# Kernel tuning notes

Hardware: AMD Instinct MI355X
Metric: run time of the kernel (lower is better)

The kernel has to match this reference:

```python
import jax, jax.numpy as jnp
import numpy as np
import math

BLOCK = 4      # block_size
N_HEADS = 8
DIM = 512
COND = 512
B = 2
HWU = 32       # h = w = u
NN = 7         # 'cross' neighbors


def _layernorm(x, w, eps=1e-5):
    mu = x.mean(-1, keepdims=True)
    var = ((x - mu) ** 2).mean(-1, keepdims=True)
    return (x - mu) * jax.lax.rsqrt(var + eps) * w


def _modulate(x, shift, scale):
    return x * (1.0 + scale) + shift


def _rotate_half(x):
    x1, x2 = jnp.split(x, 2, axis=-1)
    return jnp.concatenate([-x2, x1], axis=-1)


def _rot(x, cos, sin):
    return x * cos + _rotate_half(x) * sin


def setup_inputs() -> dict:
    key = jax.random.key(0)
    ks = jax.random.split(key, 16)
    h = w = u = HWU
    S = h * w * u
    dh = DIM // N_HEADS
    P = BLOCK ** 3
    ib = HWU // BLOCK                       # blocks per axis = 8
    nb = ib ** 3                            # 512 blocks per batch

    x = jax.random.normal(ks[0], (B, S, DIM), jnp.float32)
    c = jax.random.normal(ks[1], (B, COND), jnp.float32)

    # proper rotary tables over P block-local positions
    inv = 1.0 / (10000.0 ** (np.arange(0, dh, 2, dtype=np.float32) / dh))
    f = np.arange(P, dtype=np.float32)[:, None] * inv[None, :]
    emb = np.concatenate([f, f], axis=-1)          # [P, dh]
    cos = jnp.asarray(np.cos(emb))[None, :, None, :]
    sin = jnp.asarray(np.sin(emb))[None, :, None, :]

    # neighbor indices (cross pattern) on the block grid, mirroring get_neighbor_indices
    grid = np.stack(np.meshgrid(np.arange(B), np.arange(ib), np.arange(ib), np.arange(ib), indexing='ij'), axis=-1)
    shifts = np.array([[0, 0, 0, 0], [0, 0, -1, 0], [0, -1, 0, 0], [0, 0, 0, -1],
                       [0, 0, 1, 0], [0, 1, 0, 0], [0, 0, 0, 1]])
    nbr = grid[..., None, :] + shifts[None, None, None, None, :, :]
    nbr[..., 1:] = np.clip(nbr[..., 1:], 0, ib - 1)
    flat = (nbr[..., 0] * ib * ib * ib + nbr[..., 1] * ib * ib
            + nbr[..., 2] * ib + nbr[..., 3]).reshape(B * nb, NN)
    # every other block is 'nonzero' -> Nsel = 512
    nonzero_blocks = np.arange(0, B * nb, 2, dtype=np.int64)
    nonzero_blocks_neighbor = flat[nonzero_blocks].reshape(-1).astype(np.int64)

    s = 0.02
    params = dict(
        norm1_w=jnp.ones((DIM,), jnp.float32),
        qkv_w=s * jax.random.normal(ks[2], (3 * DIM, DIM), jnp.float32),
        out_w=s * jax.random.normal(ks[3], (DIM, DIM), jnp.float32),
        norm2_w=jnp.ones((DIM,), jnp.float32),
        mlp_w1=s * jax.random.normal(ks[4], (4 * DIM, DIM), jnp.float32),
        mlp_b1=jnp.zeros((4 * DIM,), jnp.float32),
        mlp_w2=s * jax.random.normal(ks[5], (DIM, 4 * DIM), jnp.float32),
        mlp_b2=jnp.zeros((DIM,), jnp.float32),
        adaln_w=s * jax.random.normal(ks[6], (6 * DIM, COND), jnp.float32),
        adaln_b=jnp.zeros((6 * DIM,), jnp.float32),
        kv_empty=s * jax.random.normal(ks[7], (1, P, 2 * DIM), jnp.float32),
    )
    return dict(x=x, c=c, cos_q=cos, sin_q=sin, cos_k=cos, sin_k=sin,
                nonzero_blocks=jnp.asarray(nonzero_blocks),
                nonzero_blocks_neighbor=jnp.asarray(nonzero_blocks_neighbor),
                h=h, w=w, u=u, **params)


def reference(x, c, cos_q, sin_q, cos_k, sin_k, nonzero_blocks, nonzero_blocks_neighbor,
              h, w, u, norm1_w, qkv_w, out_w, norm2_w, mlp_w1, mlp_b1, mlp_w2, mlp_b2,
              adaln_w, adaln_b, kv_empty):
    Bx, S, D = x.shape
    bs = BLOCK
    ix, iy, iz = h // bs, w // bs, u // bs
    nb = ix * iy * iz
    P = bs ** 3
    dh = D // N_HEADS
    Nsel = nonzero_blocks.shape[0]

    def transform(t):
        t = t.reshape(Bx, ix, bs, iy, bs, iz, bs, D)
        return t.transpose(0, 1, 3, 5, 2, 4, 6, 7).reshape(Bx, nb, P, D)

    def inverse_transform(t):
        t = t.reshape(Bx, ix, iy, iz, bs, bs, bs, D)
        return t.transpose(0, 1, 4, 2, 5, 3, 6, 7).reshape(Bx, S, D)

    mods = (c @ adaln_w.T + adaln_b)[:, None, :]         # [B,1,6D]
    shift_msa, scale_msa, gate_msa, shift_mlp, scale_mlp, gate_mlp = jnp.split(mods, 6, axis=-1)

    x_skip = x
    xm = _modulate(_layernorm(x, norm1_w), shift_msa, scale_msa)
    xb = transform(xm).reshape(Bx * nb, P, D)
    x_sel = xb[nonzero_blocks]                            # [Nsel,P,D]

    qkv = x_sel @ qkv_w.T                                 # [Nsel,P,3D]
    q, k, v = jnp.split(qkv, 3, axis=-1)
    k_e, v_e = jnp.split(kv_empty, 2, axis=-1)            # [1,P,D]
    k_full = jnp.broadcast_to(k_e, (Bx * nb, P, D)).at[nonzero_blocks].set(k)
    v_full = jnp.broadcast_to(v_e, (Bx * nb, P, D)).at[nonzero_blocks].set(v)
    kn = k_full[nonzero_blocks_neighbor]                  # [Nsel*NN,P,D]
    vn = v_full[nonzero_blocks_neighbor]

    qh = _rot(q.reshape(Nsel, P, N_HEADS, dh), cos_q, sin_q)
    kh = _rot(kn.reshape(Nsel * NN, P, N_HEADS, dh), cos_k, sin_k)
    kh = kh.reshape(Nsel, NN * P, N_HEADS, dh)
    vh = vn.reshape(Nsel, NN * P, N_HEADS, dh)

    scores = jnp.einsum('bqhd,bkhd->bhqk', qh, kh) / math.sqrt(dh)
    attn = jax.nn.softmax(scores, axis=-1)
    out = jnp.einsum('bhqk,bkhd->bqhd', attn, vh).reshape(Nsel, P, D)

    xz = jnp.zeros((Bx * nb, P, D), out.dtype).at[nonzero_blocks].set(out)
    x_attn = inverse_transform(xz.reshape(Bx, nb, P, D))
    x1 = x_skip + gate_msa * (x_attn @ out_w.T)

    x2 = _modulate(_layernorm(x1, norm2_w), shift_mlp, scale_mlp)
    mlp = jax.nn.gelu(x2 @ mlp_w1.T + mlp_b1, approximate=True) @ mlp_w2.T + mlp_b2
    return x1 + gate_mlp * mlp
```

## Files before the change

### kernel.cpp

```cpp
#include <hip/hip_runtime.h>
#include <cstdint>
#include <cstddef>

typedef unsigned short u16;
typedef __attribute__((ext_vector_type(8))) __bf16 bf16x8;
typedef __attribute__((ext_vector_type(4))) float f32x4;

typedef __attribute__((address_space(1))) const void GAS;
typedef __attribute__((address_space(3))) void LAS;

__device__ __forceinline__ void gld_lds16(const void* g, void* l) {
  __builtin_amdgcn_global_load_lds((GAS*)g, (LAS*)l, 16, 0, 0);
}

__device__ __forceinline__ u16 f2bf(float f) {
  union { float f; unsigned u; } x; x.f = f;
  unsigned r = x.u + 0x7FFFu + ((x.u >> 16) & 1u);
  return (u16)(r >> 16);
}
__device__ __forceinline__ float bf2f(u16 s) {
  union { unsigned u; float f; } x; x.u = ((unsigned)s) << 16;
  return x.f;
}
__device__ __forceinline__ f32x4 mfma16(bf16x8 a, bf16x8 b, f32x4 c) {
  return __builtin_amdgcn_mfma_f32_16x16x32_bf16(a, b, c, 0, 0, 0);
}


__global__ void selmap_k(const int* __restrict__ nzb, int* __restrict__ map) {
  int t = threadIdx.x;
  map[t] = -1;
  __syncthreads();
  if (t < 512) map[nzb[t]] = t;
}

__global__ __launch_bounds__(256) void castw_k(const float* __restrict__ in,
                                               u16* __restrict__ out, int n4) {
  int i = blockIdx.x * 256 + threadIdx.x;
  if (i >= n4) return;
  float4 v = ((const float4*)in)[i];
  u16 o[4] = {f2bf(v.x), f2bf(v.y), f2bf(v.z), f2bf(v.w)};
  ((uint2*)out)[i] = *(uint2*)o;
}

__global__ __launch_bounds__(256) void adaln_k(const float* __restrict__ c,
    const float* __restrict__ w, const float* __restrict__ b, float* __restrict__ mods) {
  int j = blockIdx.x * 256 + threadIdx.x;
  int bt = blockIdx.y;
  const float4* cr = (const float4*)(c + bt * 512);
  const float4* wr = (const float4*)(w + (size_t)j * 512);
  float s = 0.f;
  #pragma unroll 4
  for (int k = 0; k < 128; ++k) {
    float4 a = wr[k], q = cr[k];
    s += a.x * q.x + a.y * q.y + a.z * q.z + a.w * q.w;
  }
  mods[bt * 3072 + j] = s + b[j];
}

__global__ __launch_bounds__(256) void kvempty_k(const float* __restrict__ kve,
    const float* __restrict__ cT, const float* __restrict__ sT,
    u16* __restrict__ kempty, u16* __restrict__ vTempty) {
  int T = blockIdx.x * 256 + threadIdx.x;
  int h = T >> 12, p = (T >> 6) & 63, d = T & 63;
  float kv = kve[p * 1024 + h * 64 + d];
  float pv = kve[p * 1024 + h * 64 + (d ^ 32)];
  float cs = cT[p * 64 + d], sn = sT[p * 64 + d];
  float r = kv * cs + ((d < 32) ? -pv : pv) * sn;
  kempty[(h * 64 + p) * 64 + d] = f2bf(r);
  vTempty[(h * 64 + d) * 64 + p] = f2bf(kve[p * 1024 + 512 + h * 64 + d]);
}


__global__ __launch_bounds__(256) void ln1_k(const float* __restrict__ x,
    const float* __restrict__ nw, const float* __restrict__ mods,
    const int* __restrict__ nzb, u16* __restrict__ xm) {
  int row = blockIdx.x * 4 + (threadIdx.x >> 6);
  int t = threadIdx.x & 63;
  int sel = row >> 6, p = row & 63;
  int g = nzb[sel];
  int bt = g >> 9, blk = g & 511;
  int s = (blk >> 6) * 4096 + (p >> 4) * 1024 + ((blk >> 3) & 7) * 128
        + ((p >> 2) & 3) * 32 + (blk & 7) * 4 + (p & 3);
  const float* src = x + ((size_t)bt * 32768 + s) * 512;
  int d0 = t * 8;
  float4 a = *(const float4*)(src + d0);
  float4 b = *(const float4*)(src + d0 + 4);
  float v[8] = {a.x, a.y, a.z, a.w, b.x, b.y, b.z, b.w};
  float sum = 0.f, sq = 0.f;
  #pragma unroll
  for (int j = 0; j < 8; ++j) { sum += v[j]; sq += v[j] * v[j]; }
  #pragma unroll
  for (int m = 1; m < 64; m <<= 1) {
    sum += __shfl_xor(sum, m, 64);
    sq  += __shfl_xor(sq, m, 64);
  }
  float mean = sum * (1.f / 512.f);
  float var = sq * (1.f / 512.f) - mean * mean;
  float rstd = rsqrtf(var + 1e-5f);
  const float* mb = mods + bt * 3072;
  u16 o[8];
  #pragma unroll
  for (int j = 0; j < 8; ++j) {
    int d = d0 + j;
    float xn = (v[j] - mean) * rstd * nw[d];
    o[j] = f2bf(xn * (1.f + mb[512 + d]) + mb[d]);
  }
  *(uint4*)(xm + (size_t)row * 512 + d0) = *(uint4*)o;
}


template <int EPI>
__global__ __launch_bounds__(512, 2) void gemm256(const u16* __restrict__ A,
    const u16* __restrict__ W, int M, int N, int K, void* __restrict__ outp,
    const float* __restrict__ bias, const u16* __restrict__ x1,
    const float* __restrict__ mods, int rowOff, int NB) {
  __shared__ u16 L[65536];
  const int nwg = gridDim.x;
  const int cpx = nwg >> 3;
  const int tile = ((int)blockIdx.x & 7) * cpx + ((int)blockIdx.x >> 3);
  const int bm = (tile / NB) * 256, bn = (tile % NB) * 256;
  const int tid = threadIdx.x;
  const int w = tid >> 6, l = tid & 63, lr = l & 15, lg = l >> 4;
  const int wr = w >> 2, wc = w & 3;

  const u16* ga[4];
  const u16* gb[4];
  #pragma unroll
  for (int i = 0; i < 4; ++i) {
    int s = i * 512 + tid;
    int r = s >> 3, c = (s & 7) ^ (r & 7);
    ga[i] = A + (size_t)(bm + r) * K + c * 8;
    gb[i] = W + (size_t)(bn + r) * K + c * 8;
  }

  f32x4 acc[8][4];
  #pragma unroll
  for (int i = 0; i < 8; ++i)
    #pragma unroll
    for (int j = 0; j < 4; ++j) acc[i][j] = (f32x4){0.f, 0.f, 0.f, 0.f};

  auto STAGE = [&](int kt, int buf) {
    u16* lb = L + buf * 32768;
    #pragma unroll
    for (int i = 0; i < 4; ++i) {
      gld_lds16(ga[i] + (size_t)kt * 64, lb + (i * 512 + tid) * 8);
      gld_lds16(gb[i] + (size_t)kt * 64, lb + 16384 + (i * 512 + tid) * 8);
    }
  };

  auto COMPUTE = [&](int buf) {
    const u16* LA = L + buf * 32768;
    const u16* LB = LA + 16384;
    bf16x8 bf[4][2];
    #pragma unroll
    for (int nf = 0; nf < 4; ++nf) {
      int Rb = wc * 64 + nf * 16 + lr;
      const u16* pb = LB + Rb * 64;
      int sw = Rb & 7;
      bf[nf][0] = *(const bf16x8*)(pb + ((lg ^ sw) << 3));
      bf[nf][1] = *(const bf16x8*)(pb + (((lg + 4) ^ sw) << 3));
    }
    __builtin_amdgcn_s_setprio(1);
    #pragma unroll
    for (int mf = 0; mf < 8; ++mf) {
      int Ra = wr * 128 + mf * 16 + lr;
      const u16* pa = LA + Ra * 64;
      int sw = Ra & 7;
      bf16x8 a0 = *(const bf16x8*)(pa + ((lg ^ sw) << 3));
      bf16x8 a1 = *(const bf16x8*)(pa + (((lg + 4) ^ sw) << 3));
      #pragma unroll
      for (int nf = 0; nf < 4; ++nf) {
        acc[mf][nf] = mfma16(a0, bf[nf][0], acc[mf][nf]);
        acc[mf][nf] = mfma16(a1, bf[nf][1], acc[mf][nf]);
      }
    }
    __builtin_amdgcn_s_setprio(0);
  };

  const int NT = K >> 6;
  STAGE(0, 0);
  for (int t = 0; t < NT - 1; ++t) {
    STAGE(t + 1, (t + 1) & 1);
    asm volatile("s_waitcnt vmcnt(8)" ::: "memory");
    __builtin_amdgcn_s_barrier();
    asm volatile("" ::: "memory");
    COMPUTE(t & 1);
    asm volatile("" ::: "memory");
    __builtin_amdgcn_s_barrier();
  }
  asm volatile("s_waitcnt vmcnt(0)" ::: "memory");
  __builtin_amdgcn_s_barrier();
  asm volatile("" ::: "memory");
  COMPUTE((NT - 1) & 1);

  const int row0 = bm + wr * 128, col0 = bn + wc * 64;
  #pragma unroll
  for (int mf = 0; mf < 8; ++mf) {
    #pragma unroll
    for (int nf = 0; nf < 4; ++nf) {
      #pragma unroll
      for (int j = 0; j < 4; ++j) {
        int row = row0 + mf * 16 + lg * 4 + j;
        int col = col0 + nf * 16 + lr;
        float v = acc[mf][nf][j];
        if constexpr (EPI == 0) {
          ((u16*)outp)[(size_t)row * N + col] = f2bf(v);
        } else if constexpr (EPI == 1) {
          ((float*)outp)[(size_t)row * N + col] = v;
        } else if constexpr (EPI == 2) {
          v += bias[col];
          float z = 1.5957691216057308f * (v + 0.044715f * v * v * v);
          float t = 1.f - 2.f / (1.f + __expf(z));
          ((u16*)outp)[(size_t)row * N + col] = f2bf(0.5f * v * (1.f + t));
        } else {
          v += bias[col];
          int grow = rowOff + row;
          int bt = grow >> 15;
          float gate = mods[bt * 3072 + 2560 + col];
          ((float*)outp)[(size_t)grow * 512 + col] =
              bf2f(x1[(size_t)grow * 512 + col]) + gate * v;
        }
      }
    }
  }
}


__global__ __launch_bounds__(256) void ropepack_k(const u16* __restrict__ qkv,
    const float* __restrict__ cq, const float* __restrict__ sq,
    const float* __restrict__ ck, const float* __restrict__ sk,
    u16* __restrict__ qb, u16* __restrict__ kb) {
  int T = blockIdx.x * 256 + threadIdx.x;
  int row = T >> 7, oct = T & 127;
  int c0 = oct * 8;
  int sel = row >> 6, p = row & 63;
  int isk = (c0 >= 512);
  int chn = c0 & 511;
  int h = chn >> 6, d0 = chn & 63;
  int lower = (d0 < 32);
  const u16* base = qkv + (size_t)row * 1536 + (isk ? 512 : 0) + h * 64;
  u16 vm[8], vp[8];
  *(uint4*)vm = *(const uint4*)(base + d0);
  *(uint4*)vp = *(const uint4*)(base + (d0 ^ 32));
  const float* cT = (isk ? ck : cq) + p * 64 + d0;
  const float* sT = (isk ? sk : sq) + p * 64 + d0;
  float scale = isk ? 1.f : 0.125f;
  u16 o[8];
  #pragma unroll
  for (int j = 0; j < 8; ++j) {
    float a = bf2f(vm[j]), b = bf2f(vp[j]);
    float r = a * cT[j] + (lower ? -b : b) * sT[j];
    o[j] = f2bf(r * scale);
  }
  u16* dst = (isk ? kb : qb) + (((size_t)sel * 8 + h) * 64 + p) * 64 + d0;
  *(uint4*)dst = *(uint4*)o;
}


__global__ __launch_bounds__(256) void vtrans_k(const u16* __restrict__ qkv,
                                                u16* __restrict__ vT) {
  __shared__ u16 tb[64 * 65];
  int sel = blockIdx.x >> 3, h = blockIdx.x & 7;
  int tid = threadIdx.x;
  int p = tid >> 2, q16 = (tid & 3) * 16;
  const u16* src = qkv + (size_t)(sel * 64 + p) * 1536 + 1024 + h * 64 + q16;
  u16 ld[16];
  *(uint4*)&ld[0] = *(const uint4*)src;
  *(uint4*)&ld[8] = *(const uint4*)(src + 8);
  #pragma unroll
  for (int j = 0; j < 16; ++j) tb[p * 65 + q16 + j] = ld[j];
  __syncthreads();
  int d = tid >> 2, po = (tid & 3) * 16;
  u16 o[16];
  #pragma unroll
  for (int j = 0; j < 16; ++j) o[j] = tb[(po + j) * 65 + d];
  u16* dst = vT + (((size_t)sel * 8 + h) * 64 + d) * 64 + po;
  *(uint4*)dst = *(uint4*)&o[0];
  *(uint4*)(dst + 8) = *(uint4*)&o[8];
}


__global__ __launch_bounds__(256, 4) void attn_k(const u16* __restrict__ qbuf,
    const u16* __restrict__ kfull, const u16* __restrict__ vT,
    const u16* __restrict__ kempty, const u16* __restrict__ vTempty,
    const int* __restrict__ nbrs, const int* __restrict__ selmap,
    u16* __restrict__ attnout) {
  __shared__ u16 KB[2][4096];
  __shared__ u16 Pl[4][16][72];
  int bid = blockIdx.x;
  int swz = (bid & 7) * 512 + (bid >> 3);
  int sel = swz >> 3, h = swz & 7;
  int tid = threadIdx.x;
  int w = tid >> 6, l = tid & 63, lr = l & 15, lg = l >> 4;

  int mmv[7];
  #pragma unroll
  for (int n = 0; n < 7; ++n) mmv[n] = selmap[nbrs[sel * 7 + n]];

  const u16* qg = qbuf + (((size_t)sel * 8 + h) * 64 + w * 16) * 64;
  bf16x8 qf0 = *(const bf16x8*)(qg + lr * 64 + lg * 8);
  bf16x8 qf1 = *(const bf16x8*)(qg + lr * 64 + 32 + lg * 8);

  int srow = tid >> 3;
  int soff = srow * 64 + (((tid & 7) ^ (srow & 7)) << 3);
  size_t hoff = (size_t)h * 4096;

  {
    const u16* kp = (mmv[0] >= 0) ? kfull + (size_t)mmv[0] * 32768 + hoff
                                  : kempty + hoff;
    gld_lds16(kp + soff, &KB[0][w * 512]);
    gld_lds16(kp + soff + 2048, &KB[0][2048 + w * 512]);
  }

  f32x4 o[4];
  float mrun[4], lrun[4];
  #pragma unroll
  for (int ct = 0; ct < 4; ++ct) o[ct] = (f32x4){0.f, 0.f, 0.f, 0.f};
  #pragma unroll
  for (int r = 0; r < 4; ++r) { mrun[r] = -1e30f; lrun[r] = 0.f; }

  #pragma unroll
  for (int n = 0; n < 7; ++n) {
    if (n < 6) {
      const u16* kp = (mmv[n + 1] >= 0) ? kfull + (size_t)mmv[n + 1] * 32768 + hoff
                                        : kempty + hoff;
      int b = (n + 1) & 1;
      gld_lds16(kp + soff, &KB[b][w * 512]);
      gld_lds16(kp + soff + 2048, &KB[b][2048 + w * 512]);
      asm volatile("s_waitcnt vmcnt(2)" ::: "memory");
    } else {
      asm volatile("s_waitcnt vmcnt(0)" ::: "memory");
    }
    __builtin_amdgcn_s_barrier();
    __builtin_amdgcn_sched_barrier(0);

    const u16* kl = &KB[n & 1][0];
    const u16* vp = (mmv[n] >= 0) ? vT + (size_t)mmv[n] * 32768 + hoff
                                  : vTempty + hoff;
    f32x4 s4[4];
    int xr = lr & 7;
    #pragma unroll
    for (int ct = 0; ct < 4; ++ct) {
      int row = ct * 16 + lr;
      bf16x8 b0 = *(const bf16x8*)(kl + row * 64 + ((lg ^ xr) << 3));
      bf16x8 b1 = *(const bf16x8*)(kl + row * 64 + (((lg + 4) ^ xr) << 3));
      f32x4 z = (f32x4){0.f, 0.f, 0.f, 0.f};
      z = mfma16(qf0, b0, z);
      z = mfma16(qf1, b1, z);
      s4[ct] = z;
    }
    float rmax[4], sc[4], rs[4];
    #pragma unroll
    for (int r = 0; r < 4; ++r)
      rmax[r] = fmaxf(fmaxf(s4[0][r], s4[1][r]), fmaxf(s4[2][r], s4[3][r]));
    #pragma unroll
    for (int r = 0; r < 4; ++r) {
      #pragma unroll
      for (int ms = 1; ms < 16; ms <<= 1)
        rmax[r] = fmaxf(rmax[r], __shfl_xor(rmax[r], ms, 64));
      float mn = fmaxf(mrun[r], rmax[r]);
      sc[r] = __expf(mrun[r] - mn);
      mrun[r] = mn;
      rs[r] = 0.f;
    }
    #pragma unroll
    for (int ct = 0; ct < 4; ++ct)
      #pragma unroll
      for (int r = 0; r < 4; ++r) {
        float e = __expf(s4[ct][r] - mrun[r]);
        s4[ct][r] = e;
        rs[r] += e;
      }
    #pragma unroll
    for (int r = 0; r < 4; ++r) {
      #pragma unroll
      for (int ms = 1; ms < 16; ms <<= 1) rs[r] += __shfl_xor(rs[r], ms, 64);
      lrun[r] = lrun[r] * sc[r] + rs[r];
    }
    #pragma unroll
    for (int ct = 0; ct < 4; ++ct)
      #pragma unroll
      for (int r = 0; r < 4; ++r) o[ct][r] *= sc[r];
    #pragma unroll
    for (int ct = 0; ct < 4; ++ct)
      #pragma unroll
      for (int r = 0; r < 4; ++r)
        Pl[w][lg * 4 + r][ct * 16 + lr] = f2bf(s4[ct][r]);
    asm volatile("s_waitcnt lgkmcnt(0)" ::: "memory");
    __builtin_amdgcn_sched_barrier(0);
    bf16x8 pa0 = *(const bf16x8*)&Pl[w][lr][lg * 8];
    bf16x8 pa1 = *(const bf16x8*)&Pl[w][lr][32 + lg * 8];
    #pragma unroll
    for (int ct = 0; ct < 4; ++ct) {
      bf16x8 v0 = *(const bf16x8*)(vp + (ct * 16 + lr) * 64 + lg * 8);
      bf16x8 v1 = *(const bf16x8*)(vp + (ct * 16 + lr) * 64 + 32 + lg * 8);
      o[ct] = mfma16(pa0, v0, o[ct]);
      o[ct] = mfma16(pa1, v1, o[ct]);
    }
    asm volatile("" ::: "memory");
    __builtin_amdgcn_s_barrier();
    __builtin_amdgcn_sched_barrier(0);
  }

  float inv[4];
  #pragma unroll
  for (int r = 0; r < 4; ++r) inv[r] = 1.f / lrun[r];
  #pragma unroll
  for (int ct = 0; ct < 4; ++ct)
    #pragma unroll
    for (int r = 0; r < 4; ++r) {
      int p = w * 16 + lg * 4 + r;
      int d = ct * 16 + lr;
      attnout[((size_t)sel * 64 + p) * 512 + h * 64 + d] = f2bf(o[ct][r] * inv[r]);
    }
}


__global__ __launch_bounds__(256) void x1ln2_k(const float* __restrict__ x,
    const float* __restrict__ opout, const int* __restrict__ selmap,
    const float* __restrict__ mods, const float* __restrict__ nw,
    u16* __restrict__ x1, u16* __restrict__ x2) {
  int row = blockIdx.x * 4 + (threadIdx.x >> 6);
  int t = threadIdx.x & 63;
  int bt = row >> 15, s = row & 32767;
  int i1 = s >> 12, p1 = (s >> 10) & 3, i2 = (s >> 7) & 7,
      p2 = (s >> 5) & 3, i3 = (s >> 2) & 7, p3 = s & 3;
  int blk = (((i1 << 3) | i2) << 3) | i3;
  int m = selmap[(bt << 9) | blk];
  int d0 = t * 8;
  const float* src = x + (size_t)row * 512 + d0;
  float4 a = *(const float4*)src;
  float4 b = *(const float4*)(src + 4);
  float v[8] = {a.x, a.y, a.z, a.w, b.x, b.y, b.z, b.w};
  const float* mb = mods + bt * 3072;
  if (m >= 0) {
    int p = (p1 << 4) | (p2 << 2) | p3;
    const float* op = opout + ((size_t)m * 64 + p) * 512 + d0;
    float4 oa = *(const float4*)op;
    float4 ob = *(const float4*)(op + 4);
    float ov[8] = {oa.x, oa.y, oa.z, oa.w, ob.x, ob.y, ob.z, ob.w};
    #pragma unroll
    for (int j = 0; j < 8; ++j) v[j] += mb[1024 + d0 + j] * ov[j];
  }
  u16 o1[8];
  #pragma unroll
  for (int j = 0; j < 8; ++j) o1[j] = f2bf(v[j]);
  *(uint4*)(x1 + (size_t)row * 512 + d0) = *(uint4*)o1;
  float sum = 0.f, sq = 0.f;
  #pragma unroll
  for (int j = 0; j < 8; ++j) { sum += v[j]; sq += v[j] * v[j]; }
  #pragma unroll
  for (int mm = 1; mm < 64; mm <<= 1) {
    sum += __shfl_xor(sum, mm, 64);
    sq  += __shfl_xor(sq, mm, 64);
  }
  float mean = sum * (1.f / 512.f);
  float var = sq * (1.f / 512.f) - mean * mean;
  float rstd = rsqrtf(var + 1e-5f);
  u16 o[8];
  #pragma unroll
  for (int j = 0; j < 8; ++j) {
    int d = d0 + j;
    float xn = (v[j] - mean) * rstd * nw[d];
    o[j] = f2bf(xn * (1.f + mb[2048 + d]) + mb[1536 + d]);
  }
  *(uint4*)(x2 + (size_t)row * 512 + d0) = *(uint4*)o;
}


extern "C" void kernel_launch(void* const* d_in, const int* in_sizes, int n_in,
                              void* d_out, int out_size, void* d_ws, size_t ws_size,
                              hipStream_t stream) {
  const float* x    = (const float*)d_in[0];
  const float* c    = (const float*)d_in[1];
  const float* cosq = (const float*)d_in[2];
  const float* sinq = (const float*)d_in[3];
  const float* cosk = (const float*)d_in[4];
  const float* sink = (const float*)d_in[5];
  const int* nzb    = (const int*)d_in[6];
  const int* nbrs   = (const int*)d_in[7];
  const float* norm1_w = (const float*)d_in[11];
  const float* qkv_w   = (const float*)d_in[12];
  const float* out_w   = (const float*)d_in[13];
  const float* norm2_w = (const float*)d_in[14];
  const float* mlp_w1  = (const float*)d_in[15];
  const float* mlp_b1  = (const float*)d_in[16];
  const float* mlp_w2  = (const float*)d_in[17];
  const float* mlp_b2  = (const float*)d_in[18];
  const float* adaln_w = (const float*)d_in[19];
  const float* adaln_b = (const float*)d_in[20];
  const float* kv_e    = (const float*)d_in[21];
  float* outp = (float*)d_out;
  char* ws = (char*)d_ws;

  const size_t MB = 1024ull * 1024ull;
  u16*   qkvb    = (u16*)(ws + 0);
  float* opout   = (float*)(ws + 0);
  u16*   hidden  = (u16*)(ws + 0);
  u16*   xm      = (u16*)(ws + 96 * MB);
  u16*   attnout = (u16*)(ws + 96 * MB);
  u16*   qb      = (u16*)(ws + 128 * MB);
  u16*   kf      = (u16*)(ws + 160 * MB);
  u16*   vT      = (u16*)(ws + 192 * MB);
  u16*   x1      = (u16*)(ws + 256 * MB);
  u16*   x2      = (u16*)(ws + 320 * MB);
  char*  S0      = ws + 384 * MB;
  float* mods    = (float*)(S0);
  int*   selmap  = (int*)(S0 + 0x8000);
  u16*   kempty  = (u16*)(S0 + 0x10000);
  u16*   vTempty = (u16*)(S0 + 0x20000);
  u16*   qkvw_bf = (u16*)(S0 + 0x30000);
  u16*   outw_bf = qkvw_bf + (size_t)1536 * 512;
  u16*   w1_bf   = outw_bf + (size_t)512 * 512;
  u16*   w2_bf   = w1_bf + (size_t)2048 * 512;

  selmap_k<<<1, 1024, 0, stream>>>(nzb, selmap);
  adaln_k<<<dim3(12, 2), 256, 0, stream>>>(c, adaln_w, adaln_b, mods);
  castw_k<<<768, 256, 0, stream>>>(qkv_w, qkvw_bf, 1536 * 512 / 4);
  castw_k<<<256, 256, 0, stream>>>(out_w, outw_bf, 512 * 512 / 4);
  castw_k<<<1024, 256, 0, stream>>>(mlp_w1, w1_bf, 2048 * 512 / 4);
  castw_k<<<1024, 256, 0, stream>>>(mlp_w2, w2_bf, 512 * 2048 / 4);
  kvempty_k<<<128, 256, 0, stream>>>(kv_e, cosk, sink, kempty, vTempty);

  ln1_k<<<8192, 256, 0, stream>>>(x, norm1_w, mods, nzb, xm);

  gemm256<0><<<768, 512, 0, stream>>>(xm, qkvw_bf, 32768, 1536, 512, qkvb,
                                      nullptr, nullptr, nullptr, 0, 6);
  ropepack_k<<<16384, 256, 0, stream>>>(qkvb, cosq, sinq, cosk, sink, qb, kf);
  vtrans_k<<<4096, 256, 0, stream>>>(qkvb, vT);

  attn_k<<<4096, 256, 0, stream>>>(qb, kf, vT, kempty, vTempty, nbrs, selmap, attnout);

  gemm256<1><<<256, 512, 0, stream>>>(attnout, outw_bf, 32768, 512, 512, opout,
                                      nullptr, nullptr, nullptr, 0, 2);

  x1ln2_k<<<16384, 256, 0, stream>>>(x, opout, selmap, mods, norm2_w, x1, x2);

  gemm256<2><<<2048, 512, 0, stream>>>(x2, w1_bf, 65536, 2048, 512, hidden,
                                       mlp_b1, nullptr, nullptr, 0, 8);
  gemm256<3><<<512, 512, 0, stream>>>(hidden, w2_bf, 65536, 512, 2048, outp,
                                      mlp_b2, x1, mods, 0, 2);
}
```

Measured before the change: 946.6 us.

## Restructure GEMM main loop into eight-phase pipeline with split-K LDS stages

Replaces the double-buffered GEMM main loop, which did one big stage and one compute per 64-wide K tile, with an 8-phase software pipeline. Each LDS buffer is split into K-halves and A/B sub-tiles with a new 32-element swizzle. Every phase issues one partial global-to-LDS load, reads a quarter of the fragments, and runs 16 MFMAs under barriers and sched_barriers. The aim is to overlap global loads, LDS reads and MFMA work more finely and hide memory latency in all four GEMMs. The cost is many more barriers per K tile and a fragile hand-tuned waitcnt schedule, and the loop assumes NT is even.

```diff
diff --git a/kernel.cpp b/kernel.cpp
--- a/kernel.cpp
+++ b/kernel.cpp
@@ -110,8 +110,49 @@
 }
 
 
+#define STG(BUF, X, KH, KT) do {                                         \
+    u16* d_ = L + ((BUF) * 4 + (X) * 2 + (KH)) * 8192;                   \
+    gld_lds16(((X) ? gB0 : gA0) + (size_t)(KT) * 64 + (KH) * 32, d_ + dst0); \
+    gld_lds16(((X) ? gB1 : gA1) + (size_t)(KT) * 64 + (KH) * 32, d_ + dst1); \
+  } while (0)
+
+#define MF4(F, AF)                                                       \
+    acc[F][0] = mfma16(AF, bfr0, acc[F][0]);                             \
+    acc[F][1] = mfma16(AF, bfr1, acc[F][1]);                             \
+    acc[F][2] = mfma16(AF, bfr2, acc[F][2]);                             \
+    acc[F][3] = mfma16(AF, bfr3, acc[F][3]);
+
+#define PH(BUF, KH, MH, RDB, STMT, VM) do {                              \
+    const u16* pa_ = L + ((BUF) * 4 + (KH)) * 8192 + arow + (MH) * 2048; \
+    bf16x8 a0_ = *(const bf16x8*)(pa_);                                  \
+    bf16x8 a1_ = *(const bf16x8*)(pa_ + 512);                            \
+    bf16x8 a2_ = *(const bf16x8*)(pa_ + 1024);                           \
+    bf16x8 a3_ = *(const bf16x8*)(pa_ + 1536);                           \
+    if (RDB) {                                                           \
+      const u16* pb_ = L + ((BUF) * 4 + 2 + (KH)) * 8192 + brow;         \
+      bfr0 = *(const bf16x8*)(pb_);                                      \
+      bfr1 = *(const bf16x8*)(pb_ + 512);                                \
+      bfr2 = *(const bf16x8*)(pb_ + 1024);                               \
+      bfr3 = *(const bf16x8*)(pb_ + 1536);                               \
+    }                                                                    \
+    STMT;                                                                \
+    if (VM) asm volatile("s_waitcnt vmcnt(6)" ::: "memory");             \
+    __builtin_amdgcn_sched_barrier(0);                                   \
+    __builtin_amdgcn_s_barrier();                                        \
+    asm volatile("s_waitcnt lgkmcnt(0)" ::: "memory");                   \
+    __builtin_amdgcn_sched_barrier(0);                                   \
+    __builtin_amdgcn_s_setprio(1);                                       \
+    MF4((MH) * 4 + 0, a0_)                                               \
+    MF4((MH) * 4 + 1, a1_)                                               \
+    MF4((MH) * 4 + 2, a2_)                                               \
+    MF4((MH) * 4 + 3, a3_)                                               \
+    __builtin_amdgcn_s_setprio(0);                                       \
+    __builtin_amdgcn_sched_barrier(0);                                   \
+    __builtin_amdgcn_s_barrier();                                        \
+  } while (0)
+
 template <int EPI>
-__global__ __launch_bounds__(512, 2) void gemm256(const u16* __restrict__ A,
+__global__ __launch_bounds__(512, 2) void gemm8p(const u16* __restrict__ A,
     const u16* __restrict__ W, int M, int N, int K, void* __restrict__ outp,
     const float* __restrict__ bias, const u16* __restrict__ x1,
     const float* __restrict__ mods, int rowOff, int NB) {
@@ -124,75 +165,45 @@
   const int w = tid >> 6, l = tid & 63, lr = l & 15, lg = l >> 4;
   const int wr = w >> 2, wc = w & 3;
 
-  const u16* ga[4];
-  const u16* gb[4];
-  #pragma unroll
-  for (int i = 0; i < 4; ++i) {
-    int s = i * 512 + tid;
-    int r = s >> 3, c = (s & 7) ^ (r & 7);
-    ga[i] = A + (size_t)(bm + r) * K + c * 8;
-    gb[i] = W + (size_t)(bn + r) * K + c * 8;
-  }
+  const int r0 = tid >> 2, j0 = (tid & 3) ^ ((r0 >> 1) & 3);
+  const int s1 = 512 + tid;
+  const int r1 = s1 >> 2, j1 = (s1 & 3) ^ ((r1 >> 1) & 3);
+  const u16* gA0 = A + (size_t)(bm + r0) * K + j0 * 8;
+  const u16* gA1 = A + (size_t)(bm + r1) * K + j1 * 8;
+  const u16* gB0 = W + (size_t)(bn + r0) * K + j0 * 8;
+  const u16* gB1 = W + (size_t)(bn + r1) * K + j1 * 8;
+  const int dst0 = tid * 8, dst1 = (512 + tid) * 8;
+
+  const int cswz8 = ((lg ^ ((lr >> 1) & 3)) << 3);
+  const int arow = (wr * 128 + lr) * 32 + cswz8;
+  const int brow = (wc * 64 + lr) * 32 + cswz8;
 
   f32x4 acc[8][4];
   #pragma unroll
   for (int i = 0; i < 8; ++i)
     #pragma unroll
     for (int j = 0; j < 4; ++j) acc[i][j] = (f32x4){0.f, 0.f, 0.f, 0.f};
-
-  auto STAGE = [&](int kt, int buf) {
-    u16* lb = L + buf * 32768;
-    #pragma unroll
-    for (int i = 0; i < 4; ++i) {
-      gld_lds16(ga[i] + (size_t)kt * 64, lb + (i * 512 + tid) * 8);
-      gld_lds16(gb[i] + (size_t)kt * 64, lb + 16384 + (i * 512 + tid) * 8);
-    }
-  };
-
-  auto COMPUTE = [&](int buf) {
-    const u16* LA = L + buf * 32768;
-    const u16* LB = LA + 16384;
-    bf16x8 bf[4][2];
-    #pragma unroll
-    for (int nf = 0; nf < 4; ++nf) {
-      int Rb = wc * 64 + nf * 16 + lr;
-      const u16* pb = LB + Rb * 64;
-      int sw = Rb & 7;
-      bf[nf][0] = *(const bf16x8*)(pb + ((lg ^ sw) << 3));
-      bf[nf][1] = *(const bf16x8*)(pb + (((lg + 4) ^ sw) << 3));
-    }
-    __builtin_amdgcn_s_setprio(1);
-    #pragma unroll
-    for (int mf = 0; mf < 8; ++mf) {
-      int Ra = wr * 128 + mf * 16 + lr;
-      const u16* pa = LA + Ra * 64;
-      int sw = Ra & 7;
-      bf16x8 a0 = *(const bf16x8*)(pa + ((lg ^ sw) << 3));
-      bf16x8 a1 = *(const bf16x8*)(pa + (((lg + 4) ^ sw) << 3));
-      #pragma unroll
-      for (int nf = 0; nf < 4; ++nf) {
-        acc[mf][nf] = mfma16(a0, bf[nf][0], acc[mf][nf]);
-        acc[mf][nf] = mfma16(a1, bf[nf][1], acc[mf][nf]);
-      }
-    }
-    __builtin_amdgcn_s_setprio(0);
-  };
+  bf16x8 bfr0, bfr1, bfr2, bfr3;
 
   const int NT = K >> 6;
-  STAGE(0, 0);
-  for (int t = 0; t < NT - 1; ++t) {
-    STAGE(t + 1, (t + 1) & 1);
-    asm volatile("s_waitcnt vmcnt(8)" ::: "memory");
-    __builtin_amdgcn_s_barrier();
-    asm volatile("" ::: "memory");
-    COMPUTE(t & 1);
-    asm volatile("" ::: "memory");
-    __builtin_amdgcn_s_barrier();
-  }
-  asm volatile("s_waitcnt vmcnt(0)" ::: "memory");
+  STG(0, 1, 0, 0); STG(0, 0, 0, 0); STG(0, 1, 1, 0); STG(0, 0, 1, 0);
+  STG(1, 1, 0, 1); STG(1, 0, 0, 1); STG(1, 1, 1, 1);
+  asm volatile("s_waitcnt vmcnt(6)" ::: "memory");
   __builtin_amdgcn_s_barrier();
-  asm volatile("" ::: "memory");
-  COMPUTE((NT - 1) & 1);
+
+  const int NIT = NT >> 1;
+  for (int I = 0; I < NIT; ++I) {
+    const int t1 = 2 * I + 1, t2k = 2 * I + 2, t3k = 2 * I + 3;
+    const bool t2v = t2k < NT, t3v = t3k < NT;
+    PH(0, 0, 0, 1, STG(1, 0, 1, t1), 0);
+    PH(0, 0, 1, 0, if (t2v) STG(0, 1, 0, t2k), 0);
+    PH(0, 1, 0, 1, if (t2v) STG(0, 0, 0, t2k), 0);
+    PH(0, 1, 1, 0, if (t2v) STG(0, 1, 1, t2k), 1);
+    PH(1, 0, 0, 1, if (t2v) STG(0, 0, 1, t2k), 0);
+    PH(1, 0, 1, 0, if (t3v) STG(1, 1, 0, t3k), 0);
+    PH(1, 1, 0, 1, if (t3v) STG(1, 0, 0, t3k), 0);
+    PH(1, 1, 1, 0, if (t3v) STG(1, 1, 1, t3k), 1);
+  }
 
   const int row0 = bm + wr * 128, col0 = bn + wc * 64;
   #pragma unroll
@@ -525,20 +536,20 @@
 
   ln1_k<<<8192, 256, 0, stream>>>(x, norm1_w, mods, nzb, xm);
 
-  gemm256<0><<<768, 512, 0, stream>>>(xm, qkvw_bf, 32768, 1536, 512, qkvb,
-                                      nullptr, nullptr, nullptr, 0, 6);
+  gemm8p<0><<<768, 512, 0, stream>>>(xm, qkvw_bf, 32768, 1536, 512, qkvb,
+                                     nullptr, nullptr, nullptr, 0, 6);
   ropepack_k<<<16384, 256, 0, stream>>>(qkvb, cosq, sinq, cosk, sink, qb, kf);
   vtrans_k<<<4096, 256, 0, stream>>>(qkvb, vT);
 
   attn_k<<<4096, 256, 0, stream>>>(qb, kf, vT, kempty, vTempty, nbrs, selmap, attnout);
 
-  gemm256<1><<<256, 512, 0, stream>>>(attnout, outw_bf, 32768, 512, 512, opout,
-                                      nullptr, nullptr, nullptr, 0, 2);
+  gemm8p<1><<<256, 512, 0, stream>>>(attnout, outw_bf, 32768, 512, 512, opout,
+                                     nullptr, nullptr, nullptr, 0, 2);
 
   x1ln2_k<<<16384, 256, 0, stream>>>(x, opout, selmap, mods, norm2_w, x1, x2);
 
-  gemm256<2><<<2048, 512, 0, stream>>>(x2, w1_bf, 65536, 2048, 512, hidden,
-                                       mlp_b1, nullptr, nullptr, 0, 8);
-  gemm256<3><<<512, 512, 0, stream>>>(hidden, w2_bf, 65536, 512, 2048, outp,
-                                      mlp_b2, x1, mods, 0, 2);
-}
+  gemm8p<2><<<2048, 512, 0, stream>>>(x2, w1_bf, 65536, 2048, 512, hidden,
+                                      mlp_b1, nullptr, nullptr, 0, 8);
+  gemm8p<3><<<512, 512, 0, stream>>>(hidden, w2_bf, 65536, 512, 2048, outp,
+                                     mlp_b2, x1, mods, 0, 2);
+}
```

Measured after the change: 934.0 us. Within noise of the previous version (-1.3%).
